# Kernel optimization log

Measured on AMD Instinct MI355X. Metric: run time of the kernel, lower is better.

## Reference

```python
import jax, jax.numpy as jnp
import numpy as np


def conv1x1(x, w, b):
    # x: (B,C,H,W), w: (Cout,Cin), b: (Cout,) -- 1x1 conv == channel matmul
    return jnp.einsum('bchw,oc->bohw', x, w) + b[None, :, None, None]


def spatial_gate(q_feat, k_feat, scale):
    # Faithful to: matmul over flattened (B*HW, C) x (C, B*HW), then
    # max over keys, mean over the batch axis, softmax over spatial dims.
    B, C, H, W = q_feat.shape
    q = q_feat.reshape(B, C, H * W).transpose(0, 2, 1).reshape(B * H * W, C)
    k = k_feat.reshape(B, C, H * W).transpose(1, 0, 2).reshape(C, B * H * W)
    s = (q @ k).reshape(B * H * W, B, H * W)          # (BHW, B, HW)
    m = jnp.mean(jnp.max(s, axis=-1), axis=-1)        # (BHW,)
    w = jax.nn.softmax(m.reshape(B, H * W) * scale, axis=-1)
    return w.reshape(B, 1, H, W)


def setup_inputs() -> dict:
    key = jax.random.key(0)
    ks = jax.random.split(key, 10)
    C = 256
    shp = (8, C, 32, 32)
    inp = {
        'x4': jax.random.normal(ks[0], shp, jnp.float32),
        'x3': jax.random.normal(ks[1], shp, jnp.float32),
        'wq': jax.random.normal(ks[2], (C, C), jnp.float32) * 0.02,
        'bq': jnp.zeros((C,), jnp.float32),
        'wk': jax.random.normal(ks[3], (C, C), jnp.float32) * 0.02,
        'bk': jnp.zeros((C,), jnp.float32),
        'wv': jax.random.normal(ks[4], (C, C), jnp.float32) * 0.02,
        'bv': jnp.zeros((C,), jnp.float32),
        'w128': jax.random.normal(ks[5], (128, C), jnp.float32) * 0.02,
        'b128': jnp.zeros((128,), jnp.float32),
    }
    return inp


def reference(x4, x3, wq, bq, wk, bk, wv, bv, w128, b128):
    C = x4.shape[1]
    scale = 1.0 / (C ** 0.5)
    # shared QKV 1x1 convs applied to both inputs
    aq = conv1x1(x4, wq, bq)
    ak = conv1x1(x4, wk, bk)
    av = conv1x1(x4, wv, bv)
    bq_f = conv1x1(x3, wq, bq)
    bk_f = conv1x1(x3, wk, bk)
    bv_f = conv1x1(x3, wv, bv)
    # four gating branches: self-self (a), self-self (b), cross a->b, cross b->a
    a_x4 = conv1x1(spatial_gate(aq, ak, scale) * av, w128, b128)
    b_x3 = conv1x1(spatial_gate(bq_f, bk_f, scale) * bv_f, w128, b128)
    x43 = conv1x1(spatial_gate(aq, bk_f, scale) * bv_f, w128, b128)
    x34 = conv1x1(spatial_gate(bq_f, ak, scale) * av, w128, b128)
    # cat order: [x34, a_x4] then [x43, b_x3]
    ab_cat = jnp.concatenate([x34, a_x4, x43, b_x3], axis=1)  # (B,512,H,W)
    # Block2D loop: block class undefined in source; surrogate = identity
    # (ab12 = concat of the two chunks == ab_cat), applied depth=4 times.
    ab12 = ab_cat
    ab12 = ab_cat * ab12
    ab_avg = jnp.mean(ab12, axis=(2, 3), keepdims=True)        # (B,512,1,1)
    ab = jax.nn.softmax(ab_avg, axis=-1)   # softmax over size-1 axis -> ones
    final = ab * ab_cat
    return final
```

## Files before the change

kernel.cpp:

```cpp
#include <hip/hip_runtime.h>

typedef unsigned short ushort_t;
typedef unsigned char uchar_t;
typedef unsigned long u64_t;
typedef __attribute__((ext_vector_type(8))) short bf16x8;
typedef __attribute__((ext_vector_type(4))) float f32x4;
typedef __attribute__((ext_vector_type(16))) float f32x16;

__device__ __forceinline__ unsigned short f2bf(float f) {
  union { float f; unsigned int u; } v; v.f = f;
  unsigned int r = v.u + 0x7FFFu + ((v.u >> 16) & 1u);
  return (unsigned short)(r >> 16);
}

__device__ __forceinline__ float bf2f(unsigned short u) {
  union { unsigned int i; float f; } v; v.i = ((unsigned int)u) << 16;
  return v.f;
}

__device__ __forceinline__ void gl_lds16(const void* gsrc, void* ldst) {
  __builtin_amdgcn_global_load_lds(
      (const __attribute__((address_space(1))) void*)gsrc,
      (__attribute__((address_space(3))) void*)ldst, 16, 0, 0);
}

__device__ __forceinline__ f32x16 zero16() {
  f32x16 z;
  #pragma unroll
  for (int i = 0; i < 16; i++) z[i] = 0.f;
  return z;
}

__device__ __forceinline__ int frag_idx(int oc, int ci) {
  return (((oc>>4)*8 + (ci>>5))<<9) + ((((ci>>3)&3)*16 + (oc&15))<<3) + (ci&7);
}

__global__ __launch_bounds__(256) void k1_weights(
    const float* __restrict__ wq, const float* __restrict__ bq,
    const float* __restrict__ wk, const float* __restrict__ bk,
    const float* __restrict__ wv, const float* __restrict__ bv,
    const float* __restrict__ w128,
    ushort_t* __restrict__ Wf, float* __restrict__ bias_all)
{
  const int ci = threadIdx.x;
  if (blockIdx.x < 512) {
    const int oc = blockIdx.x;
    const float v = (oc < 256) ? wq[oc*256 + ci] : wk[(oc-256)*256 + ci];
    Wf[frag_idx(oc, ci)] = f2bf(v);
    if (ci == 0) bias_all[oc] = (oc < 256) ? bq[oc] : bk[oc-256];
  } else {
    const int og = (blockIdx.x - 512) * 4;
    float a0 = 0.f, a1 = 0.f, a2 = 0.f, a3 = 0.f;
    for (int co = 0; co < 256; co++) {
      const float wvv = wv[co*256 + ci];
      a0 += w128[(og+0)*256 + co] * wvv;
      a1 += w128[(og+1)*256 + co] * wvv;
      a2 += w128[(og+2)*256 + co] * wvv;
      a3 += w128[(og+3)*256 + co] * wvv;
    }
    Wf[frag_idx(512+og+0, ci)] = f2bf(a0);
    Wf[frag_idx(512+og+1, ci)] = f2bf(a1);
    Wf[frag_idx(512+og+2, ci)] = f2bf(a2);
    Wf[frag_idx(512+og+3, ci)] = f2bf(a3);
    if (ci < 4) {
      float s = 0.f;
      for (int co = 0; co < 256; co++) s += w128[(og+ci)*256 + co] * bv[co];
      bias_all[512 + og + ci] = s;
    }
  }
}

__global__ __launch_bounds__(256) void k2_features(
    const float* __restrict__ x4, const float* __restrict__ x3,
    const ushort_t* __restrict__ Wf, const float* __restrict__ bias_all,
    uchar_t* __restrict__ Qf8, uchar_t* __restrict__ Kf8, float* __restrict__ V)
{
  __shared__ ushort_t Af[32*512];
  __shared__ ushort_t Wl[2][32*512];
  __shared__ ushort_t Lt[64*72];

  const int tid = threadIdx.x;
  const int w = tid >> 6, lane = tid & 63;
  const int mrow = lane & 15, quad = lane >> 4;
  const int ln31 = lane & 31, half = lane >> 5;

  const int px0 = blockIdx.x * 64;
  const int src = px0 >> 13, b = (px0 >> 10) & 7, hw0 = px0 & 1023;
  const float* xp = (src ? x3 : x4) + (size_t)b*262144;

  for (int kb = 0; kb < 8; kb++)
    gl_lds16(Wf + ((size_t)((0*4 + w)*8 + kb)<<9) + lane*8, &Wl[0][(w*8+kb)*512]);

  {
    const int hw = hw0 + w*16 + mrow;
    for (int kb = 0; kb < 8; kb++) {
      const int ch0 = kb*32 + quad*8;
      bf16x8 pk;
      #pragma unroll
      for (int j = 0; j < 8; j++)
        ((ushort_t*)&pk)[j] = f2bf(xp[(size_t)(ch0 + j)*1024 + hw]);
      *(bf16x8*)&Af[(w*8 + kb)*512 + lane*8] = pk;
    }
  }
  __syncthreads();

  for (int ot = 0; ot < 10; ot++) {
    const int nbuf = (ot+1) & 1, cbuf = ot & 1;
    if (ot < 9)
      for (int kb = 0; kb < 8; kb++)
        gl_lds16(Wf + ((size_t)(((ot+1)*4 + w)*8 + kb)<<9) + lane*8,
                 &Wl[nbuf][(w*8+kb)*512]);
    asm volatile("s_waitcnt vmcnt(8)" ::: "memory");

    f32x4 acc[4];
    #pragma unroll
    for (int lg = 0; lg < 4; lg++) acc[lg] = (f32x4){0.f,0.f,0.f,0.f};
    #pragma unroll
    for (int kb = 0; kb < 8; kb++) {
      const bf16x8 a = *(const bf16x8*)&Wl[cbuf][(w*8 + kb)*512 + lane*8];
      #pragma unroll
      for (int lg = 0; lg < 4; lg++) {
        const bf16x8 bx = *(const bf16x8*)&Af[(lg*8 + kb)*512 + lane*8];
        acc[lg] = __builtin_amdgcn_mfma_f32_16x16x32_bf16(a, bx, acc[lg], 0, 0, 0);
      }
    }
    const int ocl = w*16 + quad*4;
    const float4 bias4 = *(const float4*)&bias_all[ot*64 + ocl];

    if (ot < 8) {
      __syncthreads();
      #pragma unroll
      for (int lg = 0; lg < 4; lg++) {
        const int px = lg*16 + mrow;
        ushort4 pk;
        pk.x = f2bf(acc[lg][0] + bias4.x);
        pk.y = f2bf(acc[lg][1] + bias4.y);
        pk.z = f2bf(acc[lg][2] + bias4.z);
        pk.w = f2bf(acc[lg][3] + bias4.w);
        *(ushort4*)&Lt[px*72 + ocl] = pk;
      }
      __syncthreads();
      const int g = w >> 1, e = w & 1;
      const int row = g*32 + ln31;
      const ushort_t* lp = &Lt[row*72 + e*32 + half*8];
      float fl[8], fh[8];
      #pragma unroll
      for (int j = 0; j < 8; j++) { fl[j] = bf2f(lp[j]); fh[j] = bf2f(lp[16+j]); }
      int w0 = __builtin_amdgcn_cvt_pk_fp8_f32(fl[0], fl[1], 0, 0);
      w0     = __builtin_amdgcn_cvt_pk_fp8_f32(fl[2], fl[3], w0, 1);
      int w1 = __builtin_amdgcn_cvt_pk_fp8_f32(fl[4], fl[5], 0, 0);
      w1     = __builtin_amdgcn_cvt_pk_fp8_f32(fl[6], fl[7], w1, 1);
      int w2 = __builtin_amdgcn_cvt_pk_fp8_f32(fh[0], fh[1], 0, 0);
      w2     = __builtin_amdgcn_cvt_pk_fp8_f32(fh[2], fh[3], w2, 1);
      int w3 = __builtin_amdgcn_cvt_pk_fp8_f32(fh[4], fh[5], 0, 0);
      w3     = __builtin_amdgcn_cvt_pk_fp8_f32(fh[6], fh[7], w3, 1);
      uchar_t* dst = (ot < 4) ? Qf8 : Kf8;
      const size_t chunk = (size_t)((px0>>5) + g)*8 + (ot&3)*2 + e;
      int4 pk4; pk4.x = w0; pk4.y = w1; pk4.z = w2; pk4.w = w3;
      *(int4*)(dst + (chunk<<10) + lane*16) = pk4;
    } else {
      const int ocv0 = (ot-8)*64 + ocl;
      float* vb = V + (((size_t)(src*8 + b)*128) << 10) + hw0;
      #pragma unroll
      for (int lg = 0; lg < 4; lg++) {
        vb[(size_t)(ocv0+0)*1024 + lg*16 + mrow] = acc[lg][0] + bias4.x;
        vb[(size_t)(ocv0+1)*1024 + lg*16 + mrow] = acc[lg][1] + bias4.y;
        vb[(size_t)(ocv0+2)*1024 + lg*16 + mrow] = acc[lg][2] + bias4.z;
        vb[(size_t)(ocv0+3)*1024 + lg*16 + mrow] = acc[lg][3] + bias4.w;
      }
    }
  }
}

__global__ __launch_bounds__(256, 2) void k3_smax(
    const uchar_t* __restrict__ Qf8, const uchar_t* __restrict__ Kf8,
    float* __restrict__ Pm)
{
  __shared__ __align__(16) uchar_t Kl[2][16384];

  const int tid = threadIdx.x;
  const int bt = blockIdx.x >> 6;
  const int rt = blockIdx.x & 63;
  const int w = tid >> 6, lane = tid & 63;
  const int ln31 = lane & 31, half = lane >> 5;

  const int rgb = rt*8 + w*2;
  const int g0 = (blockIdx.x & 1) * 8;

  #pragma unroll
  for (int q = 0; q < 4; q++) {
    const int c = w*4 + q;
    gl_lds16(Kf8 + (((size_t)(bt*32 + g0*2 + (c>>3))*8 + (c&7))<<10) + lane*16,
             &Kl[0][c*1024]);
  }

  u64_t qf[2][16];
  #pragma unroll
  for (int rg = 0; rg < 2; rg++)
    #pragma unroll
    for (int kp = 0; kp < 8; kp++) {
      const ulonglong2 qv = *(const ulonglong2*)(
          Qf8 + (((size_t)(rgb + rg)*8 + kp)<<10) + lane*16);
      qf[rg][2*kp] = qv.x; qf[rg][2*kp+1] = qv.y;
    }

  f32x16 rmax0, rmax1;
  #pragma unroll
  for (int i = 0; i < 16; i++) { rmax0[i] = -3.4e38f; rmax1[i] = -3.4e38f; }

  for (int s = 0; s < 16; s++) {
    __syncthreads();
    if (s < 15) {
      const int gn = (s + 1 + g0) & 15;
      #pragma unroll
      for (int q = 0; q < 4; q++) {
        const int c = w*4 + q;
        gl_lds16(Kf8 + (((size_t)(bt*32 + gn*2 + (c>>3))*8 + (c&7))<<10) + lane*16,
                 &Kl[(s+1)&1][c*1024]);
      }
    }
    const uchar_t* kl = Kl[s & 1];
    #pragma unroll
    for (int cgl = 0; cgl < 2; cgl++) {
      f32x16 a0 = zero16(), a1 = zero16();
      #pragma unroll
      for (int kp = 0; kp < 8; kp++) {
        const ulonglong2 kc = *(const ulonglong2*)&kl[(cgl*8 + kp)*1024 + lane*16];
        a0 = __builtin_amdgcn_mfma_f32_32x32x16_fp8_fp8((long)qf[0][2*kp],   (long)kc.x, a0, 0, 0, 0);
        a1 = __builtin_amdgcn_mfma_f32_32x32x16_fp8_fp8((long)qf[1][2*kp],   (long)kc.x, a1, 0, 0, 0);
        a0 = __builtin_amdgcn_mfma_f32_32x32x16_fp8_fp8((long)qf[0][2*kp+1], (long)kc.y, a0, 0, 0, 0);
        a1 = __builtin_amdgcn_mfma_f32_32x32x16_fp8_fp8((long)qf[1][2*kp+1], (long)kc.y, a1, 0, 0, 0);
      }
      #pragma unroll
      for (int i = 0; i < 16; i++) {
        rmax0[i] = fmaxf(rmax0[i], a0[i]);
        rmax1[i] = fmaxf(rmax1[i], a1[i]);
      }
    }
  }

  #pragma unroll
  for (int rg = 0; rg < 2; rg++) {
    #pragma unroll
    for (int e = 0; e < 16; e++) {
      float v = (rg == 0) ? rmax0[e] : rmax1[e];
      v = fmaxf(v, __shfl_xor(v, 1));
      v = fmaxf(v, __shfl_xor(v, 2));
      v = fmaxf(v, __shfl_xor(v, 4));
      v = fmaxf(v, __shfl_xor(v, 8));
      v = fmaxf(v, __shfl_xor(v, 16));
      if (ln31 == 0) {
        const int row = rt*256 + w*64 + rg*32 + (e&3) + 8*(e>>2) + 4*half;
        Pm[(size_t)bt*16384 + row] = v;
      }
    }
  }
}

__global__ __launch_bounds__(1024) void k4_gates(
    const float* __restrict__ Pm, float* __restrict__ G)
{
  __shared__ float red[1024];
  const int tid = threadIdx.x;
  const int qset = blockIdx.x >> 3, b = blockIdx.x & 7;
  const int i = qset*8192 + b*1024 + tid;

  float ma = 0.f, mb = 0.f;
  #pragma unroll
  for (int bt = 0; bt < 8; bt++)  ma += Pm[(size_t)bt*16384 + i];
  #pragma unroll
  for (int bt = 8; bt < 16; bt++) mb += Pm[(size_t)bt*16384 + i];
  const float sc = 0.125f * 0.0625f;
  const float la = ma * sc, lb = mb * sc;

  red[tid] = la; __syncthreads();
  for (int s = 512; s > 0; s >>= 1) { if (tid < s) red[tid] = fmaxf(red[tid], red[tid+s]); __syncthreads(); }
  const float Ma = red[0]; __syncthreads();
  const float ea = expf(la - Ma);
  red[tid] = ea; __syncthreads();
  for (int s = 512; s > 0; s >>= 1) { if (tid < s) red[tid] += red[tid+s]; __syncthreads(); }
  const float ga = ea / red[0]; __syncthreads();

  red[tid] = lb; __syncthreads();
  for (int s = 512; s > 0; s >>= 1) { if (tid < s) red[tid] = fmaxf(red[tid], red[tid+s]); __syncthreads(); }
  const float Mb = red[0]; __syncthreads();
  const float eb = expf(lb - Mb);
  red[tid] = eb; __syncthreads();
  for (int s = 512; s > 0; s >>= 1) { if (tid < s) red[tid] += red[tid+s]; __syncthreads(); }
  const float gb = eb / red[0];

  G[(size_t)(qset*2 + 0)*8192 + b*1024 + tid] = ga;
  G[(size_t)(qset*2 + 1)*8192 + b*1024 + tid] = gb;
}

__global__ __launch_bounds__(256) void k5_out(
    const float* __restrict__ V, const float* __restrict__ G,
    const float* __restrict__ b128, float* __restrict__ out)
{
  const int idx = blockIdx.x*256 + threadIdx.x;
  const int flat = idx << 2;
  const int hw = flat & 1023;
  const int ch = (flat >> 10) & 511;
  const int b  = flat >> 19;
  const int blk = ch >> 7, o = ch & 127;
  const int gidx = (blk == 0) ? 2 : (blk == 1) ? 0 : (blk == 2) ? 1 : 3;
  const int src = (blk >= 2) ? 1 : 0;

  const float4 v = *(const float4*)&V[((size_t)((src*8 + b)*128 + o) << 10) + hw];
  const float4 g = *(const float4*)&G[(size_t)gidx*8192 + b*1024 + hw];
  const float bias = b128[o];
  float4 r;
  r.x = g.x*v.x + bias; r.y = g.y*v.y + bias;
  r.z = g.z*v.z + bias; r.w = g.w*v.w + bias;
  *(float4*)&out[flat] = r;
}

extern "C" void kernel_launch(void* const* d_in, const int* in_sizes, int n_in,
                              void* d_out, int out_size, void* d_ws, size_t ws_size,
                              hipStream_t stream)
{
  const float* x4   = (const float*)d_in[0];
  const float* x3   = (const float*)d_in[1];
  const float* wq   = (const float*)d_in[2];
  const float* bq   = (const float*)d_in[3];
  const float* wk   = (const float*)d_in[4];
  const float* bk   = (const float*)d_in[5];
  const float* wv   = (const float*)d_in[6];
  const float* bv   = (const float*)d_in[7];
  const float* w128 = (const float*)d_in[8];
  const float* b128 = (const float*)d_in[9];
  float* out = (float*)d_out;

  char* ws = (char*)d_ws;
  uchar_t*  Qf8 = (uchar_t*)ws;  ws += (size_t)512*8*1024;
  uchar_t*  Kf8 = (uchar_t*)ws;  ws += (size_t)512*8*1024;
  float*    V   = (float*)ws;    ws += (size_t)2*8*128*1024*4;
  float*    Pm  = (float*)ws;    ws += (size_t)16*16384*4;
  ushort_t* Wf  = (ushort_t*)ws; ws += (size_t)640*256*2;
  float* bias_all = (float*)ws;  ws += 640*4;
  float*    G   = (float*)ws;

  k1_weights <<<544,  256, 0, stream>>>(wq, bq, wk, bk, wv, bv, w128, Wf, bias_all);
  k2_features<<<256,  256, 0, stream>>>(x4, x3, Wf, bias_all, Qf8, Kf8, V);
  k3_smax    <<<1024, 256, 0, stream>>>(Qf8, Kf8, Pm);
  k4_gates   <<<16,  1024, 0, stream>>>(Pm, G);
  k5_out     <<<4096, 256, 0, stream>>>(V, G, b128, out);
}
```

Baseline: 215.7 us.

## Use scaled 32x32x64 FP8 MFMA in score kernel and split feature projection grid

The score-max kernel swaps the 32x32x16 fp8 MFMA for the gfx950 scaled 32x32x64 f8f6f4 MFMA with unit scales, which cuts the instruction count by four. It also doubles the LDS key tile to 32KB per buffer, so there are 8 stages instead of 16. The feature kernel is split across a second grid dimension, giving each block 5 of the 10 output tiles, which doubles the block count to improve occupancy at the cost of converting the input activations twice. Doubling LDS to 64KB per block may limit how many blocks fit on a CU.

```diff
diff --git a/kernel.cpp b/kernel.cpp
--- a/kernel.cpp
+++ b/kernel.cpp
@@ -6,6 +6,7 @@
 typedef __attribute__((ext_vector_type(8))) short bf16x8;
 typedef __attribute__((ext_vector_type(4))) float f32x4;
 typedef __attribute__((ext_vector_type(16))) float f32x16;
+typedef __attribute__((ext_vector_type(8))) int v8i;
 
 __device__ __forceinline__ unsigned short f2bf(float f) {
   union { float f; unsigned int u; } v; v.f = f;
@@ -22,13 +23,6 @@
   __builtin_amdgcn_global_load_lds(
       (const __attribute__((address_space(1))) void*)gsrc,
       (__attribute__((address_space(3))) void*)ldst, 16, 0, 0);
-}
-
-__device__ __forceinline__ f32x16 zero16() {
-  f32x16 z;
-  #pragma unroll
-  for (int i = 0; i < 16; i++) z[i] = 0.f;
-  return z;
 }
 
 __device__ __forceinline__ int frag_idx(int oc, int ci) {
@@ -88,8 +82,11 @@
   const int src = px0 >> 13, b = (px0 >> 10) & 7, hw0 = px0 & 1023;
   const float* xp = (src ? x3 : x4) + (size_t)b*262144;
 
+  const int ot0 = blockIdx.y * 5;
+
   for (int kb = 0; kb < 8; kb++)
-    gl_lds16(Wf + ((size_t)((0*4 + w)*8 + kb)<<9) + lane*8, &Wl[0][(w*8+kb)*512]);
+    gl_lds16(Wf + ((size_t)((ot0*4 + w)*8 + kb)<<9) + lane*8,
+             &Wl[ot0&1][(w*8+kb)*512]);
 
   {
     const int hw = hw0 + w*16 + mrow;
@@ -104,13 +101,16 @@
   }
   __syncthreads();
 
-  for (int ot = 0; ot < 10; ot++) {
+  for (int ot = ot0; ot < ot0 + 5; ot++) {
     const int nbuf = (ot+1) & 1, cbuf = ot & 1;
-    if (ot < 9)
+    if (ot + 1 < ot0 + 5) {
       for (int kb = 0; kb < 8; kb++)
         gl_lds16(Wf + ((size_t)(((ot+1)*4 + w)*8 + kb)<<9) + lane*8,
                  &Wl[nbuf][(w*8+kb)*512]);
-    asm volatile("s_waitcnt vmcnt(8)" ::: "memory");
+      asm volatile("s_waitcnt vmcnt(8)" ::: "memory");
+    } else {
+      asm volatile("s_waitcnt vmcnt(0)" ::: "memory");
+    }
 
     f32x4 acc[4];
     #pragma unroll
@@ -176,7 +176,7 @@
     const uchar_t* __restrict__ Qf8, const uchar_t* __restrict__ Kf8,
     float* __restrict__ Pm)
 {
-  __shared__ __align__(16) uchar_t Kl[2][16384];
+  __shared__ __align__(16) uchar_t Kl[2][32768];
 
   const int tid = threadIdx.x;
   const int bt = blockIdx.x >> 6;
@@ -185,51 +185,64 @@
   const int ln31 = lane & 31, half = lane >> 5;
 
   const int rgb = rt*8 + w*2;
-  const int g0 = (blockIdx.x & 1) * 8;
-
-  #pragma unroll
-  for (int q = 0; q < 4; q++) {
-    const int c = w*4 + q;
-    gl_lds16(Kf8 + (((size_t)(bt*32 + g0*2 + (c>>3))*8 + (c&7))<<10) + lane*16,
-             &Kl[0][c*1024]);
-  }
-
-  u64_t qf[2][16];
+  const int ph = (blockIdx.x & 1)*4;
+
+  #pragma unroll
+  for (int q = 0; q < 8; q++) {
+    const int c = w*8 + q;
+    const int cg = bt*32 + ph*4 + (c>>3);
+    gl_lds16(Kf8 + (((size_t)cg*8 + (c&7))<<10) + lane*16, &Kl[0][c*1024]);
+  }
+
+  v8i qa[2][4];
   #pragma unroll
   for (int rg = 0; rg < 2; rg++)
     #pragma unroll
-    for (int kp = 0; kp < 8; kp++) {
-      const ulonglong2 qv = *(const ulonglong2*)(
-          Qf8 + (((size_t)(rgb + rg)*8 + kp)<<10) + lane*16);
-      qf[rg][2*kp] = qv.x; qf[rg][2*kp+1] = qv.y;
-    }
-
-  f32x16 rmax0, rmax1;
+    for (int u = 0; u < 4; u++) {
+      const int4 p0 = *(const int4*)(Qf8 + (((size_t)(rgb + rg)*8 + 2*u+0)<<10) + lane*16);
+      const int4 p1 = *(const int4*)(Qf8 + (((size_t)(rgb + rg)*8 + 2*u+1)<<10) + lane*16);
+      qa[rg][u] = (v8i){p0.x, p0.y, p0.z, p0.w, p1.x, p1.y, p1.z, p1.w};
+    }
+
+  f32x16 zv;
+  #pragma unroll
+  for (int i = 0; i < 16; i++) zv[i] = 0.f;
+  f32x16 rmax0 = zv, rmax1 = zv;
   #pragma unroll
   for (int i = 0; i < 16; i++) { rmax0[i] = -3.4e38f; rmax1[i] = -3.4e38f; }
 
-  for (int s = 0; s < 16; s++) {
+  for (int s = 0; s < 8; s++) {
     __syncthreads();
-    if (s < 15) {
-      const int gn = (s + 1 + g0) & 15;
-      #pragma unroll
-      for (int q = 0; q < 4; q++) {
-        const int c = w*4 + q;
-        gl_lds16(Kf8 + (((size_t)(bt*32 + gn*2 + (c>>3))*8 + (c&7))<<10) + lane*16,
+    if (s < 7) {
+      const int sn = (s + 1 + ph) & 7;
+      #pragma unroll
+      for (int q = 0; q < 8; q++) {
+        const int c = w*8 + q;
+        const int cg = bt*32 + sn*4 + (c>>3);
+        gl_lds16(Kf8 + (((size_t)cg*8 + (c&7))<<10) + lane*16,
                  &Kl[(s+1)&1][c*1024]);
       }
     }
     const uchar_t* kl = Kl[s & 1];
     #pragma unroll
-    for (int cgl = 0; cgl < 2; cgl++) {
-      f32x16 a0 = zero16(), a1 = zero16();
-      #pragma unroll
-      for (int kp = 0; kp < 8; kp++) {
-        const ulonglong2 kc = *(const ulonglong2*)&kl[(cgl*8 + kp)*1024 + lane*16];
-        a0 = __builtin_amdgcn_mfma_f32_32x32x16_fp8_fp8((long)qf[0][2*kp],   (long)kc.x, a0, 0, 0, 0);
-        a1 = __builtin_amdgcn_mfma_f32_32x32x16_fp8_fp8((long)qf[1][2*kp],   (long)kc.x, a1, 0, 0, 0);
-        a0 = __builtin_amdgcn_mfma_f32_32x32x16_fp8_fp8((long)qf[0][2*kp+1], (long)kc.y, a0, 0, 0, 0);
-        a1 = __builtin_amdgcn_mfma_f32_32x32x16_fp8_fp8((long)qf[1][2*kp+1], (long)kc.y, a1, 0, 0, 0);
+    for (int cgl = 0; cgl < 4; cgl++) {
+      v8i bu[4];
+      #pragma unroll
+      for (int u = 0; u < 4; u++) {
+        const int4 b0 = *(const int4*)&kl[(cgl*8 + 2*u+0)*1024 + lane*16];
+        const int4 b1 = *(const int4*)&kl[(cgl*8 + 2*u+1)*1024 + lane*16];
+        bu[u] = (v8i){b0.x, b0.y, b0.z, b0.w, b1.x, b1.y, b1.z, b1.w};
+      }
+      f32x16 a0 = __builtin_amdgcn_mfma_scale_f32_32x32x64_f8f6f4(
+          qa[0][0], bu[0], zv, 0, 0, 0, 0x7F7F7F7F, 0, 0x7F7F7F7F);
+      f32x16 a1 = __builtin_amdgcn_mfma_scale_f32_32x32x64_f8f6f4(
+          qa[1][0], bu[0], zv, 0, 0, 0, 0x7F7F7F7F, 0, 0x7F7F7F7F);
+      #pragma unroll
+      for (int u = 1; u < 4; u++) {
+        a0 = __builtin_amdgcn_mfma_scale_f32_32x32x64_f8f6f4(
+            qa[0][u], bu[u], a0, 0, 0, 0, 0x7F7F7F7F, 0, 0x7F7F7F7F);
+        a1 = __builtin_amdgcn_mfma_scale_f32_32x32x64_f8f6f4(
+            qa[1][u], bu[u], a1, 0, 0, 0, 0x7F7F7F7F, 0, 0x7F7F7F7F);
       }
       #pragma unroll
       for (int i = 0; i < 16; i++) {
@@ -340,9 +353,9 @@
   float* bias_all = (float*)ws;  ws += 640*4;
   float*    G   = (float*)ws;
 
-  k1_weights <<<544,  256, 0, stream>>>(wq, bq, wk, bk, wv, bv, w128, Wf, bias_all);
-  k2_features<<<256,  256, 0, stream>>>(x4, x3, Wf, bias_all, Qf8, Kf8, V);
-  k3_smax    <<<1024, 256, 0, stream>>>(Qf8, Kf8, Pm);
-  k4_gates   <<<16,  1024, 0, stream>>>(Pm, G);
-  k5_out     <<<4096, 256, 0, stream>>>(V, G, b128, out);
-}
+  k1_weights <<<544,          256, 0, stream>>>(wq, bq, wk, bk, wv, bv, w128, Wf, bias_all);
+  k2_features<<<dim3(256, 2), 256, 0, stream>>>(x4, x3, Wf, bias_all, Qf8, Kf8, V);
+  k3_smax    <<<1024,         256, 0, stream>>>(Qf8, Kf8, Pm);
+  k4_gates   <<<16,          1024, 0, stream>>>(Pm, G);
+  k5_out     <<<4096,         256, 0, stream>>>(V, G, b128, out);
+}
```

Result: faster. 204.2 us (-5.4%).
